# Kernel optimization log

Measured on AMD Instinct MI355X. Metric: run time of the kernel, lower is better.

The kernel has to match this reference:

```python
import jax, jax.numpy as jnp
import numpy as np

N = 50000      # nodes
E = 800000     # edges (before self-loops)
DIN = 256
HID = 64
HEADS = 4
DOUT = 128
NEG_SLOPE = 0.2  # PyG GATConv default leaky-relu slope


def setup_inputs() -> dict:
    key = jax.random.key(0)
    ks = jax.random.split(key, 10)
    s = 0.05
    x = jax.random.normal(ks[0], (N, DIN), jnp.float32)
    edge_index = jax.random.randint(ks[1], (2, E), 0, N, dtype=jnp.int32)
    W1 = jax.random.normal(ks[2], (DIN, HEADS * HID), jnp.float32) * s
    a1_src = jax.random.normal(ks[3], (HEADS, HID), jnp.float32) * s
    a1_dst = jax.random.normal(ks[4], (HEADS, HID), jnp.float32) * s
    b1 = jnp.zeros((HEADS * HID,), jnp.float32)
    W2 = jax.random.normal(ks[5], (HEADS * HID, DOUT), jnp.float32) * s
    a2_src = jax.random.normal(ks[6], (1, DOUT), jnp.float32) * s
    a2_dst = jax.random.normal(ks[7], (1, DOUT), jnp.float32) * s
    b2 = jnp.zeros((DOUT,), jnp.float32)
    return {"x": x, "edge_index": edge_index,
            "W1": W1, "a1_src": a1_src, "a1_dst": a1_dst, "b1": b1,
            "W2": W2, "a2_src": a2_src, "a2_dst": a2_dst, "b2": b2}


def _gat_conv(x, src, dst, W, a_src, a_dst, b, heads, concat):
    """PyG-style GATConv (self-loops already appended to src/dst)."""
    n = x.shape[0]
    h = (x @ W).reshape(n, heads, -1)               # [N, H, C]
    e_src = jnp.einsum('nhc,hc->nh', h, a_src)       # [N, H]
    e_dst = jnp.einsum('nhc,hc->nh', h, a_dst)
    logits = jax.nn.leaky_relu(e_src[src] + e_dst[dst], NEG_SLOPE)  # [E', H]
    # segment softmax over incoming edges of each dst node
    m = jax.ops.segment_max(logits, dst, num_segments=n)
    ex = jnp.exp(logits - m[dst])
    denom = jax.ops.segment_sum(ex, dst, num_segments=n)
    alpha = ex / (denom[dst] + 1e-16)                # [E', H]
    msg = alpha[:, :, None] * h[src]                 # [E', H, C]
    out = jax.ops.segment_sum(msg, dst, num_segments=n)  # [N, H, C]
    if concat:
        out = out.reshape(n, -1)
    else:
        out = out.mean(axis=1)
    return out + b


def reference(x, edge_index, W1, a1_src, a1_dst, b1, W2, a2_src, a2_dst, b2):
    n = x.shape[0]
    loop = jnp.arange(n, dtype=edge_index.dtype)
    src = jnp.concatenate([edge_index[0], loop])
    dst = jnp.concatenate([edge_index[1], loop])
    h = jax.nn.elu(_gat_conv(x, src, dst, W1, a1_src, a1_dst, b1, HEADS, True))
    h = jax.nn.elu(_gat_conv(h, src, dst, W2, a2_src, a2_dst, b2, 1, False))
    return h.mean(axis=1)  # [N]
```

## Files before the change

kernel.cpp:

```cpp
#include <hip/hip_runtime.h>
#include <math.h>

#define N_NODES 50000
#define M_PAD   50048
#define N_EDGES 800000
#define EP (N_EDGES + N_NODES)
#define DIN 256
#define HEADS 4
#define HID 64
#define F1 256
#define F2 128
#define NEG_SLOPE 0.2f
#define SCAN_NBLK ((N_NODES + 255)/256)

typedef short bf16x8 __attribute__((ext_vector_type(8)));
typedef float f32x4  __attribute__((ext_vector_type(4)));

static __device__ __forceinline__ float leaky(float x){ return x > 0.f ? x : NEG_SLOPE*x; }
static __device__ __forceinline__ float elu_f(float x){ return x > 0.f ? x : (__expf(x)-1.f); }
static __device__ __forceinline__ float b2f(unsigned short u){ return __uint_as_float(((unsigned)u)<<16); }
static __device__ __forceinline__ unsigned short f2b(float f){
  unsigned u = __float_as_uint(f);
  return (unsigned short)((u + 0x7fffu + ((u>>16)&1u)) >> 16);
}

__global__ __launch_bounds__(256) void k_hist(const int* __restrict__ dst, int* __restrict__ counts){
  int e = blockIdx.x*256 + threadIdx.x;
  if (e >= EP) return;
  int d = (e < N_EDGES) ? dst[e] : (e - N_EDGES);
  atomicAdd(&counts[d], 1);
}

__global__ __launch_bounds__(256) void k_scan1(const int* __restrict__ counts,
                                               int* __restrict__ exc, int* __restrict__ bsum){
  int i = blockIdx.x*256 + threadIdx.x;
  int v = (i < N_NODES) ? counts[i] : 0;
  int lane = threadIdx.x & 63, wave = threadIdx.x >> 6;
  int inc = v;
  #pragma unroll
  for (int off=1; off<64; off<<=1){
    int n = __shfl_up(inc, off);
    if (lane >= off) inc += n;
  }
  __shared__ int wsum[4];
  if (lane == 63) wsum[wave] = inc;
  __syncthreads();
  int wpre = 0;
  #pragma unroll
  for (int w=0; w<4; w++) if (w < wave) wpre += wsum[w];
  if (i < N_NODES) exc[i] = wpre + inc - v;
  if (threadIdx.x == 255) bsum[blockIdx.x] = wpre + inc;
}

__global__ __launch_bounds__(256) void k_scan2(const int* __restrict__ bsum,
                                               int* __restrict__ bpref, int* __restrict__ offsets){
  int i = threadIdx.x;
  int v = (i < SCAN_NBLK) ? bsum[i] : 0;
  int lane = threadIdx.x & 63, wave = threadIdx.x >> 6;
  int inc = v;
  #pragma unroll
  for (int off=1; off<64; off<<=1){
    int n = __shfl_up(inc, off);
    if (lane >= off) inc += n;
  }
  __shared__ int wsum[4];
  if (lane == 63) wsum[wave] = inc;
  __syncthreads();
  int wpre = 0;
  #pragma unroll
  for (int w=0; w<4; w++) if (w < wave) wpre += wsum[w];
  if (i < SCAN_NBLK) bpref[i] = wpre + inc - v;
  if (i == 255) offsets[N_NODES] = wpre + inc;
}

__global__ __launch_bounds__(256) void k_scan3(const int* __restrict__ exc, const int* __restrict__ bpref,
                                               int* __restrict__ offsets, int* __restrict__ cursor){
  int i = blockIdx.x*256 + threadIdx.x;
  if (i >= N_NODES) return;
  int o = exc[i] + bpref[blockIdx.x];
  offsets[i] = o;
  cursor[i] = o;
}

__global__ __launch_bounds__(256) void k_scatter(const int* __restrict__ src, const int* __restrict__ dst,
                          int* __restrict__ cursor, int* __restrict__ sorted_src){
  int e = blockIdx.x*256 + threadIdx.x;
  if (e >= EP) return;
  int s, d;
  if (e < N_EDGES){ s = src[e]; d = dst[e]; } else { s = d = e - N_EDGES; }
  int pos = atomicAdd(&cursor[d], 1);
  sorted_src[pos] = s;
}

__global__ __launch_bounds__(256) void k_dhist(const int* __restrict__ counts,
                                               int* __restrict__ dbin, int* __restrict__ bcount){
  __shared__ int h[256];
  h[threadIdx.x] = 0;
  __syncthreads();
  int i = blockIdx.x*256 + threadIdx.x;
  if (i < N_NODES){
    int b = counts[i]; if (b > 255) b = 255;
    atomicAdd(&h[b], 1);
  }
  __syncthreads();
  int c = h[threadIdx.x];
  bcount[(size_t)blockIdx.x*256 + threadIdx.x] = c;
  if (c) atomicAdd(&dbin[threadIdx.x], c);
}

__global__ __launch_bounds__(256) void k_dscan(const int* __restrict__ dbin, int* __restrict__ dbase){
  int i = threadIdx.x;
  int v = dbin[i];
  int lane = threadIdx.x & 63, wave = threadIdx.x >> 6;
  int inc = v;
  #pragma unroll
  for (int off=1; off<64; off<<=1){
    int n = __shfl_up(inc, off);
    if (lane >= off) inc += n;
  }
  __shared__ int wsum[4];
  if (lane == 63) wsum[wave] = inc;
  __syncthreads();
  int wpre = 0;
  #pragma unroll
  for (int w=0; w<4; w++) if (w < wave) wpre += wsum[w];
  dbase[i] = wpre + inc - v;
}

__global__ __launch_bounds__(256) void k_dcol(const int* __restrict__ bcount, const int* __restrict__ dbase,
                                              int* __restrict__ colbase){
  int bin = threadIdx.x;
  int run = dbase[bin];
  for (int blk=0; blk<SCAN_NBLK; blk++){
    colbase[(size_t)blk*256 + bin] = run;
    run += bcount[(size_t)blk*256 + bin];
  }
}

__global__ __launch_bounds__(256) void k_dscatter(const int* __restrict__ counts, const int* __restrict__ colbase,
                                                  int* __restrict__ perm){
  __shared__ int h[256];
  h[threadIdx.x] = 0;
  __syncthreads();
  int i = blockIdx.x*256 + threadIdx.x;
  if (i < N_NODES){
    int b = counts[i]; if (b > 255) b = 255;
    int r = atomicAdd(&h[b], 1);
    perm[colbase[(size_t)blockIdx.x*256 + b] + r] = i;
  }
}

__global__ __launch_bounds__(256) void k_splitA(const float* __restrict__ X,
                         unsigned short* __restrict__ Ahi){
  int gid = blockIdx.x*256 + threadIdx.x;
  size_t base = (size_t)gid*4;
  int row = (int)(base >> 8);
  ushort4 hi;
  if (row < N_NODES){
    float4 v = *(const float4*)(X + base);
    hi.x=f2b(v.x); hi.y=f2b(v.y); hi.z=f2b(v.z); hi.w=f2b(v.w);
  } else {
    hi = {0,0,0,0};
  }
  *(ushort4*)(Ahi + base) = hi;
}

__global__ __launch_bounds__(256) void k_splitWT(const float* __restrict__ W,
                          unsigned short* __restrict__ Bhi, int Kd, int Nd){
  int t = blockIdx.x*256 + threadIdx.x;
  if (t >= Kd*Nd) return;
  int n = t / Kd, k = t % Kd;
  Bhi[(size_t)n*Kd + k] = f2b(W[(size_t)k*Nd + n]);
}

__global__ __launch_bounds__(256) void k_gemm1f(
    const unsigned short* __restrict__ A, const unsigned short* __restrict__ Bt,
    const float* __restrict__ a1s, const float* __restrict__ a1d,
    unsigned short* __restrict__ Cbf, float* __restrict__ es, float* __restrict__ ed){
  const int K = 256, Nc = F1;
  int tid = threadIdx.x;
  int wave = tid>>6, lane = tid&63;
  int wc = wave;
  int row0 = blockIdx.x*64;
  int col0 = wc*64;
  int lrow = lane&15, lk = (lane>>4)*8;
  f32x4 acc[4][4] = {};
  bf16x8 aA[4], bA[4], aB[4], bB[4];
  auto LOADF = [&](bf16x8* av, bf16x8* bv, int KS){
    #pragma unroll
    for (int i=0;i<4;i++){
      av[i] = *(const bf16x8*)(A  + (size_t)(row0 + i*16 + lrow)*K + KS + lk);
      bv[i] = *(const bf16x8*)(Bt + (size_t)(col0 + i*16 + lrow)*K + KS + lk);
    }
  };
  auto MFMAS = [&](bf16x8* av, bf16x8* bv){
    #pragma unroll
    for (int i=0;i<4;i++)
      #pragma unroll
      for (int j=0;j<4;j++)
        acc[i][j] = __builtin_amdgcn_mfma_f32_16x16x32_bf16(av[i], bv[j], acc[i][j], 0,0,0);
  };
  LOADF(aA,bA,0);
  #pragma unroll
  for (int ks=0; ks<K; ks+=64){
    LOADF(aB,bB,ks+32);
    MFMAS(aA,bA);
    if (ks+64 < K) LOADF(aA,bA,ks+64);
    MFMAS(aB,bB);
  }
  int crow = (lane>>4)*4, ccol = lane&15;
  #pragma unroll
  for (int i=0;i<4;i++)
    #pragma unroll
    for (int j=0;j<4;j++)
      #pragma unroll
      for (int q=0;q<4;q++){
        int r = row0 + i*16 + crow + q;
        int c = col0 + j*16 + ccol;
        Cbf[(size_t)r*Nc + c] = f2b(acc[i][j][q]);
      }
  float avs[4], avd[4];
  #pragma unroll
  for (int j=0;j<4;j++){
    avs[j] = a1s[wc*64 + j*16 + ccol];
    avd[j] = a1d[wc*64 + j*16 + ccol];
  }
  #pragma unroll
  for (int i=0;i<4;i++){
    #pragma unroll
    for (int q=0;q<4;q++){
      float ps = acc[i][0][q]*avs[0] + acc[i][1][q]*avs[1] + acc[i][2][q]*avs[2] + acc[i][3][q]*avs[3];
      float pd = acc[i][0][q]*avd[0] + acc[i][1][q]*avd[1] + acc[i][2][q]*avd[2] + acc[i][3][q]*avd[3];
      #pragma unroll
      for (int off=1; off<16; off<<=1){ ps += __shfl_xor(ps,off); pd += __shfl_xor(pd,off); }
      if ((lane&15)==0){
        int r = row0 + i*16 + crow + q;
        es[(size_t)r*4 + wc] = ps;
        ed[(size_t)r*4 + wc] = pd;
      }
    }
  }
}

template<int WR, int WC>
__global__ __launch_bounds__(256) void k_gemm_bf(
    const unsigned short* __restrict__ A, const unsigned short* __restrict__ Bt,
    unsigned short* __restrict__ Cbf, int Nc){
  const int K = 256;
  int tid = threadIdx.x;
  int wave = tid>>6, lane = tid&63;
  int wr = wave / WC, wc = wave % WC;
  int row0 = blockIdx.x*(WR*64) + wr*64;
  int col0 = blockIdx.y*(WC*64) + wc*64;
  int lrow = lane&15, lk = (lane>>4)*8;
  f32x4 acc[4][4] = {};
  bf16x8 aA[4], bA[4], aB[4], bB[4];
  auto LOADF = [&](bf16x8* av, bf16x8* bv, int KS){
    #pragma unroll
    for (int i=0;i<4;i++){
      av[i] = *(const bf16x8*)(A  + (size_t)(row0 + i*16 + lrow)*K + KS + lk);
      bv[i] = *(const bf16x8*)(Bt + (size_t)(col0 + i*16 + lrow)*K + KS + lk);
    }
  };
  auto MFMAS = [&](bf16x8* av, bf16x8* bv){
    #pragma unroll
    for (int i=0;i<4;i++)
      #pragma unroll
      for (int j=0;j<4;j++)
        acc[i][j] = __builtin_amdgcn_mfma_f32_16x16x32_bf16(av[i], bv[j], acc[i][j], 0,0,0);
  };
  LOADF(aA,bA,0);
  #pragma unroll
  for (int ks=0; ks<K; ks+=64){
    LOADF(aB,bB,ks+32);
    MFMAS(aA,bA);
    if (ks+64 < K) LOADF(aA,bA,ks+64);
    MFMAS(aB,bB);
  }
  int crow = (lane>>4)*4, ccol = lane&15;
  #pragma unroll
  for (int i=0;i<4;i++)
    #pragma unroll
    for (int j=0;j<4;j++)
      #pragma unroll
      for (int q=0;q<4;q++){
        int r = row0 + i*16 + crow + q;
        int c = col0 + j*16 + ccol;
        Cbf[(size_t)r*Nc + c] = f2b(acc[i][j][q]);
      }
}

__global__ __launch_bounds__(256) void k_edot2(const unsigned short* __restrict__ h2bf, const float* __restrict__ a_src,
                        const float* __restrict__ a_dst, float* __restrict__ es, float* __restrict__ ed){
  int wave=threadIdx.x>>6, lane=threadIdx.x&63;
  int n = blockIdx.x*4+wave; if (n>=N_NODES) return;
  ushort2 hv = ((const ushort2*)(h2bf + (size_t)n*F2))[lane];
  float2 s2 = ((const float2*)a_src)[lane];
  float2 d2 = ((const float2*)a_dst)[lane];
  float h0=b2f(hv.x), h1=b2f(hv.y);
  float ps = h0*s2.x + h1*s2.y;
  float pd = h0*d2.x + h1*d2.y;
  #pragma unroll
  for (int m=1;m<64;m<<=1){ ps += __shfl_xor(ps,m); pd += __shfl_xor(pd,m); }
  if (lane==0){ es[n]=ps; ed[n]=pd; }
}

__global__ __launch_bounds__(256) void k_agg1(const unsigned short* __restrict__ h1bf, const float* __restrict__ es,
                       const float* __restrict__ ed, const int* __restrict__ offsets,
                       const int* __restrict__ ssrc, const int* __restrict__ perm,
                       const float* __restrict__ b1,
                       unsigned short* __restrict__ A2hi){
  int wave = threadIdx.x>>6, lane = threadIdx.x&63;
  int idx = blockIdx.x*4 + wave;
  if (idx >= M_PAD) return;
  if (idx >= N_NODES){
    ushort4 z = {0,0,0,0};
    ((ushort4*)(A2hi + (size_t)idx*F1))[lane] = z;
    return;
  }
  int d = perm[idx];
  int beg = offsets[d], end = offsets[d+1];
  int deg = end - beg;
  float4 edv = *(const float4*)(ed + (size_t)d*4);
  int head = lane>>4;
  float edh = head==0?edv.x:(head==1?edv.y:(head==2?edv.z:edv.w));
  float s0=0.f,s1=0.f,s2=0.f,s3=0.f;
  float4 acc0={0,0,0,0}, acc1={0,0,0,0}, acc2={0,0,0,0}, acc3={0,0,0,0};
  int j=0;
  for (; j+4<=deg; j+=4){
    int sn0=ssrc[beg+j], sn1=ssrc[beg+j+1], sn2=ssrc[beg+j+2], sn3=ssrc[beg+j+3];
    float e0 = es[(size_t)sn0*4+head], e1 = es[(size_t)sn1*4+head];
    float e2 = es[(size_t)sn2*4+head], e3 = es[(size_t)sn3*4+head];
    ushort4 v0 = ((const ushort4*)(h1bf + (size_t)sn0*F1))[lane];
    ushort4 v1 = ((const ushort4*)(h1bf + (size_t)sn1*F1))[lane];
    ushort4 v2 = ((const ushort4*)(h1bf + (size_t)sn2*F1))[lane];
    ushort4 v3 = ((const ushort4*)(h1bf + (size_t)sn3*F1))[lane];
    float x0 = __expf(leaky(e0+edh)), x1 = __expf(leaky(e1+edh));
    float x2 = __expf(leaky(e2+edh)), x3 = __expf(leaky(e3+edh));
    s0+=x0; s1+=x1; s2+=x2; s3+=x3;
    acc0.x=fmaf(x0,b2f(v0.x),acc0.x); acc0.y=fmaf(x0,b2f(v0.y),acc0.y); acc0.z=fmaf(x0,b2f(v0.z),acc0.z); acc0.w=fmaf(x0,b2f(v0.w),acc0.w);
    acc1.x=fmaf(x1,b2f(v1.x),acc1.x); acc1.y=fmaf(x1,b2f(v1.y),acc1.y); acc1.z=fmaf(x1,b2f(v1.z),acc1.z); acc1.w=fmaf(x1,b2f(v1.w),acc1.w);
    acc2.x=fmaf(x2,b2f(v2.x),acc2.x); acc2.y=fmaf(x2,b2f(v2.y),acc2.y); acc2.z=fmaf(x2,b2f(v2.z),acc2.z); acc2.w=fmaf(x2,b2f(v2.w),acc2.w);
    acc3.x=fmaf(x3,b2f(v3.x),acc3.x); acc3.y=fmaf(x3,b2f(v3.y),acc3.y); acc3.z=fmaf(x3,b2f(v3.z),acc3.z); acc3.w=fmaf(x3,b2f(v3.w),acc3.w);
  }
  for (; j<deg; j++){
    int sn=ssrc[beg+j];
    float e = es[(size_t)sn*4+head];
    ushort4 v = ((const ushort4*)(h1bf + (size_t)sn*F1))[lane];
    float x = __expf(leaky(e+edh));
    s0 += x;
    acc0.x=fmaf(x,b2f(v.x),acc0.x); acc0.y=fmaf(x,b2f(v.y),acc0.y);
    acc0.z=fmaf(x,b2f(v.z),acc0.z); acc0.w=fmaf(x,b2f(v.w),acc0.w);
  }
  float inv = 1.f/(s0+s1+s2+s3+1e-16f);
  float4 acc;
  acc.x = (acc0.x+acc1.x+acc2.x+acc3.x)*inv;
  acc.y = (acc0.y+acc1.y+acc2.y+acc3.y)*inv;
  acc.z = (acc0.z+acc1.z+acc2.z+acc3.z)*inv;
  acc.w = (acc0.w+acc1.w+acc2.w+acc3.w)*inv;
  float4 bb = *(const float4*)(b1 + lane*4);
  ushort4 hi;
  hi.x = f2b(elu_f(acc.x + bb.x));
  hi.y = f2b(elu_f(acc.y + bb.y));
  hi.z = f2b(elu_f(acc.z + bb.z));
  hi.w = f2b(elu_f(acc.w + bb.w));
  ((ushort4*)(A2hi + (size_t)d*F1))[lane] = hi;
}

__global__ __launch_bounds__(256) void k_agg2(const unsigned short* __restrict__ h2bf, const float* __restrict__ es,
                       const float* __restrict__ ed, const int* __restrict__ offsets,
                       const int* __restrict__ ssrc, const int* __restrict__ perm,
                       const float* __restrict__ b2, float* __restrict__ out){
  int wave=threadIdx.x>>6, lane=threadIdx.x&63;
  int idx = blockIdx.x*4+wave; if (idx>=N_NODES) return;
  int d = perm[idx];
  int beg=offsets[d], end=offsets[d+1];
  int deg=end-beg;
  float edv = ed[d];
  float s0=0.f,s1=0.f,s2=0.f,s3=0.f;
  float2 acc0={0,0}, acc1={0,0}, acc2={0,0}, acc3={0,0};
  int j=0;
  for (; j+4<=deg; j+=4){
    int sn0=ssrc[beg+j], sn1=ssrc[beg+j+1], sn2=ssrc[beg+j+2], sn3=ssrc[beg+j+3];
    float e0=es[sn0], e1=es[sn1], e2=es[sn2], e3=es[sn3];
    ushort2 v0 = ((const ushort2*)(h2bf + (size_t)sn0*F2))[lane];
    ushort2 v1 = ((const ushort2*)(h2bf + (size_t)sn1*F2))[lane];
    ushort2 v2 = ((const ushort2*)(h2bf + (size_t)sn2*F2))[lane];
    ushort2 v3 = ((const ushort2*)(h2bf + (size_t)sn3*F2))[lane];
    float x0=__expf(leaky(e0+edv)), x1=__expf(leaky(e1+edv));
    float x2=__expf(leaky(e2+edv)), x3=__expf(leaky(e3+edv));
    s0+=x0; s1+=x1; s2+=x2; s3+=x3;
    acc0.x=fmaf(x0,b2f(v0.x),acc0.x); acc0.y=fmaf(x0,b2f(v0.y),acc0.y);
    acc1.x=fmaf(x1,b2f(v1.x),acc1.x); acc1.y=fmaf(x1,b2f(v1.y),acc1.y);
    acc2.x=fmaf(x2,b2f(v2.x),acc2.x); acc2.y=fmaf(x2,b2f(v2.y),acc2.y);
    acc3.x=fmaf(x3,b2f(v3.x),acc3.x); acc3.y=fmaf(x3,b2f(v3.y),acc3.y);
  }
  for (; j<deg; j++){
    int sn=ssrc[beg+j];
    float x = __expf(leaky(es[sn]+edv));
    ushort2 v = ((const ushort2*)(h2bf + (size_t)sn*F2))[lane];
    s0 += x;
    acc0.x=fmaf(x,b2f(v.x),acc0.x); acc0.y=fmaf(x,b2f(v.y),acc0.y);
  }
  float inv = 1.f/(s0+s1+s2+s3+1e-16f);
  float2 acc;
  acc.x = (acc0.x+acc1.x+acc2.x+acc3.x)*inv;
  acc.y = (acc0.y+acc1.y+acc2.y+acc3.y)*inv;
  float2 bb = *(const float2*)(b2 + lane*2);
  float r = elu_f(acc.x+bb.x) + elu_f(acc.y+bb.y);
  #pragma unroll
  for (int off=1;off<64;off<<=1) r += __shfl_xor(r,off);
  if (lane==0) out[d] = r * (1.f/128.f);
}

extern "C" void kernel_launch(void* const* d_in, const int* in_sizes, int n_in,
                              void* d_out, int out_size, void* d_ws, size_t ws_size,
                              hipStream_t stream) {
  const float* x   = (const float*)d_in[0];
  const int*   ei  = (const int*)d_in[1];
  const int*   esrc = ei;
  const int*   edst = ei + N_EDGES;
  const float* W1  = (const float*)d_in[2];
  const float* a1s = (const float*)d_in[3];
  const float* a1d = (const float*)d_in[4];
  const float* b1  = (const float*)d_in[5];
  const float* W2  = (const float*)d_in[6];
  const float* a2s = (const float*)d_in[7];
  const float* a2d = (const float*)d_in[8];
  const float* b2  = (const float*)d_in[9];
  float* out = (float*)d_out;

  char* ws = (char*)d_ws;
  size_t off = 0;
  auto alloc = [&](size_t bytes)->void*{ void* p = ws + off; off += (bytes + 255) & ~(size_t)255; return p; };
  unsigned short* A1hi = (unsigned short*)alloc((size_t)M_PAD*F1*2);
  unsigned short* h1bf = (unsigned short*)alloc((size_t)M_PAD*F1*2);
  unsigned short* h2bf = (unsigned short*)alloc((size_t)M_PAD*F2*2);
  unsigned short* Bt1hi= (unsigned short*)alloc((size_t)F1*DIN*2);
  unsigned short* Bt2hi= (unsigned short*)alloc((size_t)F2*F1*2);
  float* e1s   = (float*)alloc((size_t)M_PAD*HEADS*4);
  float* e1d   = (float*)alloc((size_t)M_PAD*HEADS*4);
  float* e2s   = (float*)alloc((size_t)N_NODES*4);
  float* e2d   = (float*)alloc((size_t)N_NODES*4);
  int*   counts= (int*)alloc((size_t)N_NODES*4);
  int*   offs  = (int*)alloc((size_t)(N_NODES+1)*4);
  int*   cursor= (int*)alloc((size_t)N_NODES*4);
  int*   exc   = (int*)alloc((size_t)N_NODES*4);
  int*   bsum  = (int*)alloc((size_t)SCAN_NBLK*4);
  int*   bpref = (int*)alloc((size_t)SCAN_NBLK*4);
  int*   perm  = (int*)alloc((size_t)N_NODES*4);
  int*   dbin  = (int*)alloc((size_t)256*4);
  int*   dbase = (int*)alloc((size_t)256*4);
  int*   bcount= (int*)alloc((size_t)SCAN_NBLK*256*4);
  int*   colbase=(int*)alloc((size_t)SCAN_NBLK*256*4);
  int*   ssrc  = (int*)alloc((size_t)EP*4);
  unsigned short* A2hi = A1hi;

  hipMemsetAsync(counts, 0, (size_t)N_NODES*4, stream);
  hipMemsetAsync(dbin, 0, (size_t)256*4, stream);
  k_hist<<<(EP+255)/256, 256, 0, stream>>>(edst, counts);
  k_scan1<<<SCAN_NBLK, 256, 0, stream>>>(counts, exc, bsum);
  k_scan2<<<1, 256, 0, stream>>>(bsum, bpref, offs);
  k_scan3<<<SCAN_NBLK, 256, 0, stream>>>(exc, bpref, offs, cursor);
  k_scatter<<<(EP+255)/256, 256, 0, stream>>>(esrc, edst, cursor, ssrc);
  k_dhist<<<SCAN_NBLK, 256, 0, stream>>>(counts, dbin, bcount);
  k_dscan<<<1, 256, 0, stream>>>(dbin, dbase);
  k_dcol<<<1, 256, 0, stream>>>(bcount, dbase, colbase);
  k_dscatter<<<SCAN_NBLK, 256, 0, stream>>>(counts, colbase, perm);

  k_splitA<<<(M_PAD*F1/4 + 255)/256, 256, 0, stream>>>(x, A1hi);
  k_splitWT<<<(DIN*F1 + 255)/256, 256, 0, stream>>>(W1, Bt1hi, DIN, F1);
  k_splitWT<<<(F1*F2 + 255)/256, 256, 0, stream>>>(W2, Bt2hi, F1, F2);

  k_gemm1f<<<M_PAD/64, 256, 0, stream>>>(A1hi, Bt1hi, a1s, a1d, h1bf, e1s, e1d);
  k_agg1<<<(M_PAD+3)/4, 256, 0, stream>>>(h1bf, e1s, e1d, offs, ssrc, perm, b1, A2hi);

  k_gemm_bf<2,2><<<M_PAD/128, 256, 0, stream>>>(A2hi, Bt2hi, h2bf, F2);
  k_edot2<<<(N_NODES+3)/4, 256, 0, stream>>>(h2bf, a2s, a2d, e2s, e2d);
  k_agg2<<<(N_NODES+3)/4, 256, 0, stream>>>(h2bf, e2s, e2d, offs, ssrc, perm, b2, out);
}
```

Measured before the change: 329.2 us.

## Precompute per-edge attention exponentials in separate edge-parallel kernels before aggregation

Adds a sorted destination array to the CSR scatter, plus two edge-parallel kernels that compute exp(leaky(es[src]+ed[dst])) for every edge of layers 1 and 2 and store them. The aggregation kernels then read these stored values contiguously instead of gathering es per neighbor and evaluating exp inline. It also switches many size_t index computations to 32-bit unsigned to shorten address arithmetic. In exchange it writes and re-reads about 17 MB of extra edge data and adds two kernel launches.

```diff
diff --git a/kernel.cpp b/kernel.cpp
--- a/kernel.cpp
+++ b/kernel.cpp
@@ -83,13 +83,14 @@
 }
 
 __global__ __launch_bounds__(256) void k_scatter(const int* __restrict__ src, const int* __restrict__ dst,
-                          int* __restrict__ cursor, int* __restrict__ sorted_src){
+                          int* __restrict__ cursor, int* __restrict__ sorted_src, int* __restrict__ sorted_dst){
   int e = blockIdx.x*256 + threadIdx.x;
   if (e >= EP) return;
   int s, d;
   if (e < N_EDGES){ s = src[e]; d = dst[e]; } else { s = d = e - N_EDGES; }
   int pos = atomicAdd(&cursor[d], 1);
   sorted_src[pos] = s;
+  sorted_dst[pos] = d;
 }
 
 __global__ __launch_bounds__(256) void k_dhist(const int* __restrict__ counts,
@@ -189,8 +190,8 @@
   auto LOADF = [&](bf16x8* av, bf16x8* bv, int KS){
     #pragma unroll
     for (int i=0;i<4;i++){
-      av[i] = *(const bf16x8*)(A  + (size_t)(row0 + i*16 + lrow)*K + KS + lk);
-      bv[i] = *(const bf16x8*)(Bt + (size_t)(col0 + i*16 + lrow)*K + KS + lk);
+      av[i] = *(const bf16x8*)(A  + (unsigned)(row0 + i*16 + lrow)*K + KS + lk);
+      bv[i] = *(const bf16x8*)(Bt + (unsigned)(col0 + i*16 + lrow)*K + KS + lk);
     }
   };
   auto MFMAS = [&](bf16x8* av, bf16x8* bv){
@@ -217,7 +218,7 @@
       for (int q=0;q<4;q++){
         int r = row0 + i*16 + crow + q;
         int c = col0 + j*16 + ccol;
-        Cbf[(size_t)r*Nc + c] = f2b(acc[i][j][q]);
+        Cbf[(unsigned)r*Nc + c] = f2b(acc[i][j][q]);
       }
   float avs[4], avd[4];
   #pragma unroll
@@ -235,8 +236,8 @@
       for (int off=1; off<16; off<<=1){ ps += __shfl_xor(ps,off); pd += __shfl_xor(pd,off); }
       if ((lane&15)==0){
         int r = row0 + i*16 + crow + q;
-        es[(size_t)r*4 + wc] = ps;
-        ed[(size_t)r*4 + wc] = pd;
+        es[(unsigned)r*4 + wc] = ps;
+        ed[(unsigned)r*4 + wc] = pd;
       }
     }
   }
@@ -258,8 +259,8 @@
   auto LOADF = [&](bf16x8* av, bf16x8* bv, int KS){
     #pragma unroll
     for (int i=0;i<4;i++){
-      av[i] = *(const bf16x8*)(A  + (size_t)(row0 + i*16 + lrow)*K + KS + lk);
-      bv[i] = *(const bf16x8*)(Bt + (size_t)(col0 + i*16 + lrow)*K + KS + lk);
+      av[i] = *(const bf16x8*)(A  + (unsigned)(row0 + i*16 + lrow)*K + KS + lk);
+      bv[i] = *(const bf16x8*)(Bt + (unsigned)(col0 + i*16 + lrow)*K + KS + lk);
     }
   };
   auto MFMAS = [&](bf16x8* av, bf16x8* bv){
@@ -286,7 +287,7 @@
       for (int q=0;q<4;q++){
         int r = row0 + i*16 + crow + q;
         int c = col0 + j*16 + ccol;
-        Cbf[(size_t)r*Nc + c] = f2b(acc[i][j][q]);
+        Cbf[(unsigned)r*Nc + c] = f2b(acc[i][j][q]);
       }
 }
 
@@ -294,7 +295,7 @@
                         const float* __restrict__ a_dst, float* __restrict__ es, float* __restrict__ ed){
   int wave=threadIdx.x>>6, lane=threadIdx.x&63;
   int n = blockIdx.x*4+wave; if (n>=N_NODES) return;
-  ushort2 hv = ((const ushort2*)(h2bf + (size_t)n*F2))[lane];
+  ushort2 hv = ((const ushort2*)(h2bf + (unsigned)n*F2))[lane];
   float2 s2 = ((const float2*)a_src)[lane];
   float2 d2 = ((const float2*)a_dst)[lane];
   float h0=b2f(hv.x), h1=b2f(hv.y);
@@ -305,8 +306,33 @@
   if (lane==0){ es[n]=ps; ed[n]=pd; }
 }
 
-__global__ __launch_bounds__(256) void k_agg1(const unsigned short* __restrict__ h1bf, const float* __restrict__ es,
-                       const float* __restrict__ ed, const int* __restrict__ offsets,
+__global__ __launch_bounds__(256) void k_eexp1(const int* __restrict__ ssrc, const int* __restrict__ sdst,
+                        const float* __restrict__ es, const float* __restrict__ ed,
+                        float* __restrict__ ex){
+  int e = blockIdx.x*256 + threadIdx.x;
+  if (e >= EP) return;
+  unsigned s = (unsigned)ssrc[e], d = (unsigned)sdst[e];
+  float4 ev = *(const float4*)(es + s*4);
+  float4 dv = *(const float4*)(ed + d*4);
+  float4 o;
+  o.x = __expf(leaky(ev.x+dv.x));
+  o.y = __expf(leaky(ev.y+dv.y));
+  o.z = __expf(leaky(ev.z+dv.z));
+  o.w = __expf(leaky(ev.w+dv.w));
+  *(float4*)(ex + (unsigned)e*4) = o;
+}
+
+__global__ __launch_bounds__(256) void k_eexp2(const int* __restrict__ ssrc, const int* __restrict__ sdst,
+                        const float* __restrict__ es, const float* __restrict__ ed,
+                        float* __restrict__ ex){
+  int e = blockIdx.x*256 + threadIdx.x;
+  if (e >= EP) return;
+  unsigned s = (unsigned)ssrc[e], d = (unsigned)sdst[e];
+  ex[e] = __expf(leaky(es[s] + ed[d]));
+}
+
+__global__ __launch_bounds__(256) void k_agg1(const unsigned short* __restrict__ h1bf, const float* __restrict__ ex1,
+                       const int* __restrict__ offsets,
                        const int* __restrict__ ssrc, const int* __restrict__ perm,
                        const float* __restrict__ b1,
                        unsigned short* __restrict__ A2hi){
@@ -315,28 +341,26 @@
   if (idx >= M_PAD) return;
   if (idx >= N_NODES){
     ushort4 z = {0,0,0,0};
-    ((ushort4*)(A2hi + (size_t)idx*F1))[lane] = z;
+    ((ushort4*)(A2hi + (unsigned)idx*F1))[lane] = z;
     return;
   }
   int d = perm[idx];
-  int beg = offsets[d], end = offsets[d+1];
-  int deg = end - beg;
-  float4 edv = *(const float4*)(ed + (size_t)d*4);
-  int head = lane>>4;
-  float edh = head==0?edv.x:(head==1?edv.y:(head==2?edv.z:edv.w));
+  unsigned beg = (unsigned)offsets[d], end = (unsigned)offsets[d+1];
+  unsigned deg = end - beg;
+  unsigned head = (unsigned)(lane>>4);
+  const ushort4* __restrict__ hb = (const ushort4*)h1bf;
+  const float* __restrict__ exh = ex1 + head;
   float s0=0.f,s1=0.f,s2=0.f,s3=0.f;
   float4 acc0={0,0,0,0}, acc1={0,0,0,0}, acc2={0,0,0,0}, acc3={0,0,0,0};
-  int j=0;
+  unsigned j=0;
   for (; j+4<=deg; j+=4){
-    int sn0=ssrc[beg+j], sn1=ssrc[beg+j+1], sn2=ssrc[beg+j+2], sn3=ssrc[beg+j+3];
-    float e0 = es[(size_t)sn0*4+head], e1 = es[(size_t)sn1*4+head];
-    float e2 = es[(size_t)sn2*4+head], e3 = es[(size_t)sn3*4+head];
-    ushort4 v0 = ((const ushort4*)(h1bf + (size_t)sn0*F1))[lane];
-    ushort4 v1 = ((const ushort4*)(h1bf + (size_t)sn1*F1))[lane];
-    ushort4 v2 = ((const ushort4*)(h1bf + (size_t)sn2*F1))[lane];
-    ushort4 v3 = ((const ushort4*)(h1bf + (size_t)sn3*F1))[lane];
-    float x0 = __expf(leaky(e0+edh)), x1 = __expf(leaky(e1+edh));
-    float x2 = __expf(leaky(e2+edh)), x3 = __expf(leaky(e3+edh));
+    unsigned e0=beg+j;
+    unsigned sn0=(unsigned)ssrc[e0], sn1=(unsigned)ssrc[e0+1], sn2=(unsigned)ssrc[e0+2], sn3=(unsigned)ssrc[e0+3];
+    float x0 = exh[e0*4], x1 = exh[e0*4+4], x2 = exh[e0*4+8], x3 = exh[e0*4+12];
+    ushort4 v0 = hb[sn0*64 + lane];
+    ushort4 v1 = hb[sn1*64 + lane];
+    ushort4 v2 = hb[sn2*64 + lane];
+    ushort4 v3 = hb[sn3*64 + lane];
     s0+=x0; s1+=x1; s2+=x2; s3+=x3;
     acc0.x=fmaf(x0,b2f(v0.x),acc0.x); acc0.y=fmaf(x0,b2f(v0.y),acc0.y); acc0.z=fmaf(x0,b2f(v0.z),acc0.z); acc0.w=fmaf(x0,b2f(v0.w),acc0.w);
     acc1.x=fmaf(x1,b2f(v1.x),acc1.x); acc1.y=fmaf(x1,b2f(v1.y),acc1.y); acc1.z=fmaf(x1,b2f(v1.z),acc1.z); acc1.w=fmaf(x1,b2f(v1.w),acc1.w);
@@ -344,10 +368,10 @@
     acc3.x=fmaf(x3,b2f(v3.x),acc3.x); acc3.y=fmaf(x3,b2f(v3.y),acc3.y); acc3.z=fmaf(x3,b2f(v3.z),acc3.z); acc3.w=fmaf(x3,b2f(v3.w),acc3.w);
   }
   for (; j<deg; j++){
-    int sn=ssrc[beg+j];
-    float e = es[(size_t)sn*4+head];
-    ushort4 v = ((const ushort4*)(h1bf + (size_t)sn*F1))[lane];
-    float x = __expf(leaky(e+edh));
+    unsigned e0=beg+j;
+    unsigned sn=(unsigned)ssrc[e0];
+    float x = exh[e0*4];
+    ushort4 v = hb[sn*64 + lane];
     s0 += x;
     acc0.x=fmaf(x,b2f(v.x),acc0.x); acc0.y=fmaf(x,b2f(v.y),acc0.y);
     acc0.z=fmaf(x,b2f(v.z),acc0.z); acc0.w=fmaf(x,b2f(v.w),acc0.w);
@@ -364,31 +388,30 @@
   hi.y = f2b(elu_f(acc.y + bb.y));
   hi.z = f2b(elu_f(acc.z + bb.z));
   hi.w = f2b(elu_f(acc.w + bb.w));
-  ((ushort4*)(A2hi + (size_t)d*F1))[lane] = hi;
-}
-
-__global__ __launch_bounds__(256) void k_agg2(const unsigned short* __restrict__ h2bf, const float* __restrict__ es,
-                       const float* __restrict__ ed, const int* __restrict__ offsets,
+  ((ushort4*)(A2hi + (unsigned)d*F1))[lane] = hi;
+}
+
+__global__ __launch_bounds__(256) void k_agg2(const unsigned short* __restrict__ h2bf, const float* __restrict__ ex2,
+                       const int* __restrict__ offsets,
                        const int* __restrict__ ssrc, const int* __restrict__ perm,
                        const float* __restrict__ b2, float* __restrict__ out){
   int wave=threadIdx.x>>6, lane=threadIdx.x&63;
   int idx = blockIdx.x*4+wave; if (idx>=N_NODES) return;
   int d = perm[idx];
-  int beg=offsets[d], end=offsets[d+1];
-  int deg=end-beg;
-  float edv = ed[d];
+  unsigned beg=(unsigned)offsets[d], end=(unsigned)offsets[d+1];
+  unsigned deg=end-beg;
+  const ushort2* __restrict__ hb = (const ushort2*)h2bf;
   float s0=0.f,s1=0.f,s2=0.f,s3=0.f;
   float2 acc0={0,0}, acc1={0,0}, acc2={0,0}, acc3={0,0};
-  int j=0;
+  unsigned j=0;
   for (; j+4<=deg; j+=4){
-    int sn0=ssrc[beg+j], sn1=ssrc[beg+j+1], sn2=ssrc[beg+j+2], sn3=ssrc[beg+j+3];
-    float e0=es[sn0], e1=es[sn1], e2=es[sn2], e3=es[sn3];
-    ushort2 v0 = ((const ushort2*)(h2bf + (size_t)sn0*F2))[lane];
-    ushort2 v1 = ((const ushort2*)(h2bf + (size_t)sn1*F2))[lane];
-    ushort2 v2 = ((const ushort2*)(h2bf + (size_t)sn2*F2))[lane];
-    ushort2 v3 = ((const ushort2*)(h2bf + (size_t)sn3*F2))[lane];
-    float x0=__expf(leaky(e0+edv)), x1=__expf(leaky(e1+edv));
-    float x2=__expf(leaky(e2+edv)), x3=__expf(leaky(e3+edv));
+    unsigned e0=beg+j;
+    unsigned sn0=(unsigned)ssrc[e0], sn1=(unsigned)ssrc[e0+1], sn2=(unsigned)ssrc[e0+2], sn3=(unsigned)ssrc[e0+3];
+    float x0=ex2[e0], x1=ex2[e0+1], x2=ex2[e0+2], x3=ex2[e0+3];
+    ushort2 v0 = hb[sn0*64 + lane];
+    ushort2 v1 = hb[sn1*64 + lane];
+    ushort2 v2 = hb[sn2*64 + lane];
+    ushort2 v3 = hb[sn3*64 + lane];
     s0+=x0; s1+=x1; s2+=x2; s3+=x3;
     acc0.x=fmaf(x0,b2f(v0.x),acc0.x); acc0.y=fmaf(x0,b2f(v0.y),acc0.y);
     acc1.x=fmaf(x1,b2f(v1.x),acc1.x); acc1.y=fmaf(x1,b2f(v1.y),acc1.y);
@@ -396,9 +419,10 @@
     acc3.x=fmaf(x3,b2f(v3.x),acc3.x); acc3.y=fmaf(x3,b2f(v3.y),acc3.y);
   }
   for (; j<deg; j++){
-    int sn=ssrc[beg+j];
-    float x = __expf(leaky(es[sn]+edv));
-    ushort2 v = ((const ushort2*)(h2bf + (size_t)sn*F2))[lane];
+    unsigned e0=beg+j;
+    unsigned sn=(unsigned)ssrc[e0];
+    float x = ex2[e0];
+    ushort2 v = hb[sn*64 + lane];
     s0 += x;
     acc0.x=fmaf(x,b2f(v.x),acc0.x); acc0.y=fmaf(x,b2f(v.y),acc0.y);
   }
@@ -442,6 +466,8 @@
   float* e1d   = (float*)alloc((size_t)M_PAD*HEADS*4);
   float* e2s   = (float*)alloc((size_t)N_NODES*4);
   float* e2d   = (float*)alloc((size_t)N_NODES*4);
+  float* ex1   = (float*)alloc((size_t)EP*HEADS*4);
+  float* ex2   = (float*)alloc((size_t)EP*4);
   int*   counts= (int*)alloc((size_t)N_NODES*4);
   int*   offs  = (int*)alloc((size_t)(N_NODES+1)*4);
   int*   cursor= (int*)alloc((size_t)N_NODES*4);
@@ -454,6 +480,7 @@
   int*   bcount= (int*)alloc((size_t)SCAN_NBLK*256*4);
   int*   colbase=(int*)alloc((size_t)SCAN_NBLK*256*4);
   int*   ssrc  = (int*)alloc((size_t)EP*4);
+  int*   sdst  = (int*)alloc((size_t)EP*4);
   unsigned short* A2hi = A1hi;
 
   hipMemsetAsync(counts, 0, (size_t)N_NODES*4, stream);
@@ -462,7 +489,7 @@
   k_scan1<<<SCAN_NBLK, 256, 0, stream>>>(counts, exc, bsum);
   k_scan2<<<1, 256, 0, stream>>>(bsum, bpref, offs);
   k_scan3<<<SCAN_NBLK, 256, 0, stream>>>(exc, bpref, offs, cursor);
-  k_scatter<<<(EP+255)/256, 256, 0, stream>>>(esrc, edst, cursor, ssrc);
+  k_scatter<<<(EP+255)/256, 256, 0, stream>>>(esrc, edst, cursor, ssrc, sdst);
   k_dhist<<<SCAN_NBLK, 256, 0, stream>>>(counts, dbin, bcount);
   k_dscan<<<1, 256, 0, stream>>>(dbin, dbase);
   k_dcol<<<1, 256, 0, stream>>>(bcount, dbase, colbase);
@@ -473,9 +500,11 @@
   k_splitWT<<<(F1*F2 + 255)/256, 256, 0, stream>>>(W2, Bt2hi, F1, F2);
 
   k_gemm1f<<<M_PAD/64, 256, 0, stream>>>(A1hi, Bt1hi, a1s, a1d, h1bf, e1s, e1d);
-  k_agg1<<<(M_PAD+3)/4, 256, 0, stream>>>(h1bf, e1s, e1d, offs, ssrc, perm, b1, A2hi);
+  k_eexp1<<<(EP+255)/256, 256, 0, stream>>>(ssrc, sdst, e1s, e1d, ex1);
+  k_agg1<<<(M_PAD+3)/4, 256, 0, stream>>>(h1bf, ex1, offs, ssrc, perm, b1, A2hi);
 
   k_gemm_bf<2,2><<<M_PAD/128, 256, 0, stream>>>(A2hi, Bt2hi, h2bf, F2);
   k_edot2<<<(N_NODES+3)/4, 256, 0, stream>>>(h2bf, a2s, a2d, e2s, e2d);
-  k_agg2<<<(N_NODES+3)/4, 256, 0, stream>>>(h2bf, e2s, e2d, offs, ssrc, perm, b2, out);
-}
+  k_eexp2<<<(EP+255)/256, 256, 0, stream>>>(ssrc, sdst, e2s, e2d, ex2);
+  k_agg2<<<(N_NODES+3)/4, 256, 0, stream>>>(h2bf, ex2, offs, ssrc, perm, b2, out);
+}
```

Result: no change. 323.0 us (-1.9%).
